# Kernel tuning notes

Hardware: AMD Instinct MI355X
Metric: run time of the kernel (lower is better)

The kernel has to match this reference:

```python
import jax, jax.numpy as jnp
import numpy as np

EPS = 1e-6


def _make_coord_3d(D, H, W, dtype):
    # torch make_coord_3d(flatten=False).permute(3,0,1,2): channels stacked as (x, y, z)
    lz = jnp.linspace(-1.0, 1.0, D, dtype=dtype)
    ly = jnp.linspace(-1.0, 1.0, H, dtype=dtype)
    lx = jnp.linspace(-1.0, 1.0, W, dtype=dtype)
    cz, cy, cx = jnp.meshgrid(lz, ly, lx, indexing='ij')
    return jnp.stack([cx, cy, cz], axis=0)  # [3, D, H, W]


def _trilinear_border(vol, gd, gh, gw):
    # vol: [C, D, H, W]; gd/gh/gw: [Q] normalized coords for the D/H/W axes.
    # Matches torch grid_sample(mode='bilinear', align_corners=False, padding_mode='border').
    C, D, H, W = vol.shape
    z = (gd + 1.0) * (D * 0.5) - 0.5
    y = (gh + 1.0) * (H * 0.5) - 0.5
    x = (gw + 1.0) * (W * 0.5) - 0.5
    z0 = jnp.floor(z); y0 = jnp.floor(y); x0 = jnp.floor(x)
    wz = (z - z0)[None]; wy = (y - y0)[None]; wx = (x - x0)[None]  # [1, Q]
    z0i = jnp.clip(z0.astype(jnp.int32), 0, D - 1); z1i = jnp.clip(z0.astype(jnp.int32) + 1, 0, D - 1)
    y0i = jnp.clip(y0.astype(jnp.int32), 0, H - 1); y1i = jnp.clip(y0.astype(jnp.int32) + 1, 0, H - 1)
    x0i = jnp.clip(x0.astype(jnp.int32), 0, W - 1); x1i = jnp.clip(x0.astype(jnp.int32) + 1, 0, W - 1)
    g = lambda zi, yi, xi: vol[:, zi, yi, xi]  # gather -> [C, Q]
    return (g(z0i, y0i, x0i) * (1 - wz) * (1 - wy) * (1 - wx)
            + g(z0i, y0i, x1i) * (1 - wz) * (1 - wy) * wx
            + g(z0i, y1i, x0i) * (1 - wz) * wy * (1 - wx)
            + g(z0i, y1i, x1i) * (1 - wz) * wy * wx
            + g(z1i, y0i, x0i) * wz * (1 - wy) * (1 - wx)
            + g(z1i, y0i, x1i) * wz * (1 - wy) * wx
            + g(z1i, y1i, x0i) * wz * wy * (1 - wx)
            + g(z1i, y1i, x1i) * wz * wy * wx)


def _forward(inp, coord, cell, W0, b0, W1, b1, W2, b2, W3, b3):
    feat = inp  # identity encoder: inp is the latent feature grid
    B, C, D, H, W = feat.shape
    rx = 2.0 / D / 2.0; ry = 2.0 / H / 2.0; rz = 2.0 / W / 2.0
    sizes = jnp.array([D, H, W], dtype=feat.dtype)
    feat_coord = _make_coord_3d(D, H, W, feat.dtype)  # [3, D, H, W]
    sample_b = jax.vmap(_trilinear_border, in_axes=(0, 0, 0, 0))
    sample_c = jax.vmap(_trilinear_border, in_axes=(None, 0, 0, 0))

    rel_cell = cell * sizes  # [B, Q, 3]
    cell_vol = jnp.abs(cell[..., 0] * cell[..., 1] * cell[..., 2])
    scale_sq = jnp.clip(8.0 / (cell_vol + 1e-8), 1.0, 64.0)[..., None]  # [B, Q, 1]

    def mlp(x):
        h = jax.nn.relu(x @ W0 + b0)
        h = jax.nn.relu(h @ W1 + b1)
        h = jax.nn.relu(h @ W2 + b2)
        return h @ W3 + b3

    preds, areas = [], []
    for vx in (-1, 1):
        for vy in (-1, 1):
            for vz in (-1, 1):
                shift = jnp.array([vx * rx + EPS, vy * ry + EPS, vz * rz + EPS], dtype=coord.dtype)
                c = jnp.clip(coord + shift, -1.0 + 1e-6, 1.0 - 1e-6)
                gd, gh, gw = c[..., 0], c[..., 1], c[..., 2]
                q_feat = sample_b(feat, gd, gh, gw).transpose(0, 2, 1)        # [B, Q, C]
                q_coord = sample_c(feat_coord, gd, gh, gw).transpose(0, 2, 1)  # [B, Q, 3]
                rel_coord = (coord - q_coord) * sizes
                x = jnp.concatenate([q_feat, rel_coord, rel_cell, scale_sq], axis=-1)
                preds.append(mlp(x))  # [B, Q, 1]
                areas.append(jnp.abs(rel_coord[..., 0] * rel_coord[..., 1] * rel_coord[..., 2]) + 1e-9)
    tot_area = jnp.stack(areas).sum(axis=0)
    areas = areas[::-1]  # local-ensemble diagonal-swap of areas
    ret = sum(p * (a / tot_area)[..., None] for p, a in zip(preds, areas))
    return ret


def setup_inputs() -> dict:
    key = jax.random.key(0)
    ks = jax.random.split(key, 8)
    B, C, D, Q, HID = 1, 64, 32, 131072, 256
    in_dim = C + 3 + 3 + 1  # 71
    w = lambda k, shape, fan_in: jax.random.normal(k, shape, jnp.float32) * (1.0 / np.sqrt(fan_in))
    inp = jax.random.normal(ks[0], (B, C, D, D, D), jnp.float32)
    coord = jax.random.uniform(ks[1], (B, Q, 3), jnp.float32, -1.0, 1.0)
    cell = jnp.full((B, Q, 3), 2.0 / 64.0, jnp.float32)  # uniform cell size of a 64^3 query grid
    return {
        'inp': inp, 'coord': coord, 'cell': cell,
        'W0': w(ks[2], (in_dim, HID), in_dim), 'b0': jnp.zeros((HID,), jnp.float32),
        'W1': w(ks[3], (HID, HID), HID), 'b1': jnp.zeros((HID,), jnp.float32),
        'W2': w(ks[4], (HID, HID), HID), 'b2': jnp.zeros((HID,), jnp.float32),
        'W3': w(ks[5], (HID, 1), HID), 'b3': jnp.zeros((1,), jnp.float32),
    }


def reference(inp, coord, cell, W0, b0, W1, b1, W2, b2, W3, b3):
    return _forward(inp, coord, cell, W0, b0, W1, b1, W2, b2, W3, b3)
```

## Files before the change

### kernel.cpp

```cpp
#include <hip/hip_runtime.h>

typedef __attribute__((ext_vector_type(8))) short s16x8;
typedef __attribute__((ext_vector_type(4))) float f32x4;

__device__ __forceinline__ unsigned short f2bf(float x) {
  unsigned u = __float_as_uint(x);
  u = (u + 0x7fffu + ((u >> 16) & 1u)) >> 16;
  return (unsigned short)u;
}
__device__ __forceinline__ float bflo(unsigned v) { return __uint_as_float(v << 16); }
__device__ __forceinline__ float bfhi(unsigned v) { return __uint_as_float(v & 0xffff0000u); }

#define FEAT_OFF 0
#define W0F_OFF  2097152
#define W1F_OFF  (W0F_OFF + 24576)
#define W2F_OFF  (W1F_OFF + 65536)
#define WS_TOTAL (W2F_OFF + 65536)

__global__ void liif_prep(const float* __restrict__ inp,
                          const float* __restrict__ W0,
                          const float* __restrict__ W1,
                          const float* __restrict__ W2,
                          unsigned short* __restrict__ ws) {
  int tid = blockIdx.x * 256 + threadIdx.x;
  if (tid < 2097152) {
    int pos = tid >> 6, c = tid & 63;
    ws[FEAT_OFF + tid] = f2bf(inp[c * 32768 + pos]);
  } else if (tid < W1F_OFF) {
    int e = tid - W0F_OFF;
    int j = e & 7, L = (e >> 3) & 63, nt = (e >> 9) & 15, c = e >> 13;
    int k = c * 32 + (L >> 4) * 8 + j, n = nt * 16 + (L & 15);
    ws[tid] = (k < 71) ? f2bf(W0[k * 256 + n]) : (unsigned short)0;
  } else if (tid < W2F_OFF) {
    int e = tid - W1F_OFF;
    int j = e & 7, L = (e >> 3) & 63, nt = (e >> 9) & 15, c = e >> 13;
    int k = c * 32 + (L >> 4) * 8 + j, n = nt * 16 + (L & 15);
    ws[tid] = f2bf(W1[k * 256 + n]);
  } else if (tid < WS_TOTAL) {
    int e = tid - W2F_OFF;
    int j = e & 7, L = (e >> 3) & 63, nt = (e >> 9) & 15, c = e >> 13;
    int k = c * 32 + (L >> 4) * 8 + j, n = nt * 16 + (L & 15);
    ws[tid] = f2bf(W2[k * 256 + n]);
  }
}

template<int KC>
__device__ __forceinline__ void run_layer(const unsigned short* __restrict__ Wf,
                                          const float* __restrict__ bias,
                                          const unsigned short* A, int astride,
                                          unsigned short* H,
                                          int wave, int quad, int l16, int lane) {
  f32x4 acc[4][4];
#pragma unroll
  for (int i = 0; i < 4; ++i)
#pragma unroll
    for (int j = 0; j < 4; ++j) acc[i][j] = (f32x4){0.f, 0.f, 0.f, 0.f};

#pragma unroll
  for (int c = 0; c < KC; ++c) {
    s16x8 a[4];
#pragma unroll
    for (int rt = 0; rt < 4; ++rt)
      a[rt] = *(const s16x8*)(A + (rt * 16 + l16) * astride + c * 32 + quad * 8);
#pragma unroll
    for (int ntl = 0; ntl < 4; ++ntl) {
      int nt = wave * 4 + ntl;
      s16x8 b = *(const s16x8*)(Wf + (((c * 16 + nt) * 64 + lane) << 3));
#pragma unroll
      for (int rt = 0; rt < 4; ++rt)
        acc[rt][ntl] = __builtin_amdgcn_mfma_f32_16x16x32_bf16(a[rt], b, acc[rt][ntl], 0, 0, 0);
    }
  }
  __syncthreads();
#pragma unroll
  for (int ntl = 0; ntl < 4; ++ntl) {
    int col = (wave * 4 + ntl) * 16 + l16;
    float bv = bias[col];
#pragma unroll
    for (int rt = 0; rt < 4; ++rt) {
#pragma unroll
      for (int i = 0; i < 4; ++i) {
        int r = rt * 16 + quad * 4 + i;
        float h = fmaxf(acc[rt][ntl][i] + bv, 0.0f);
        H[r * 264 + col] = f2bf(h);
      }
    }
  }
  __syncthreads();
}

__global__ __launch_bounds__(256, 3)
void liif_main(const float* __restrict__ coord,
               const float* __restrict__ cell,
               const float* __restrict__ b0,
               const float* __restrict__ b1,
               const float* __restrict__ b2,
               const float* __restrict__ W3,
               const float* __restrict__ b3,
               const unsigned short* __restrict__ ws,
               float* __restrict__ out) {
  __shared__ __align__(16) unsigned short sm_x[64 * 104];
  __shared__ __align__(16) unsigned short sm_h[64 * 264];
  __shared__ float sm_area[64];
  __shared__ float sm_pred[64];

  const unsigned short* feat = ws + FEAT_OFF;
  const int tid = threadIdx.x;
  const int lane = tid & 63;
  const int wave = tid >> 6;
  const int quad = lane >> 4;
  const int l16 = lane & 15;

  {
    const int row = tid >> 2, p = tid & 3;
    const int ql = row >> 3, s = row & 7;
    const int q = blockIdx.x * 8 + ql;
    const float c0r = coord[q * 3 + 0], c1r = coord[q * 3 + 1], c2r = coord[q * 3 + 2];
    const float R = 0.03125f;
    const float sh0 = ((s & 4) ? R : -R) + 1e-6f;
    const float sh1 = ((s & 2) ? R : -R) + 1e-6f;
    const float sh2 = ((s & 1) ? R : -R) + 1e-6f;
    const float LO = -1.0f + 1e-6f, HI = 1.0f - 1e-6f;
    float c0 = fminf(fmaxf(c0r + sh0, LO), HI);
    float c1 = fminf(fmaxf(c1r + sh1, LO), HI);
    float c2 = fminf(fmaxf(c2r + sh2, LO), HI);
    float z = (c0 + 1.0f) * 16.0f - 0.5f;
    float y = (c1 + 1.0f) * 16.0f - 0.5f;
    float x = (c2 + 1.0f) * 16.0f - 0.5f;
    float zf = floorf(z), yf = floorf(y), xf = floorf(x);
    float wz = z - zf, wy = y - yf, wx = x - xf;
    int z0 = min(max((int)zf, 0), 31), z1 = min(max((int)zf + 1, 0), 31);
    int y0 = min(max((int)yf, 0), 31), y1 = min(max((int)yf + 1, 0), 31);
    int x0 = min(max((int)xf, 0), 31), x1 = min(max((int)xf + 1, 0), 31);
    float wz0 = 1.0f - wz, wy0 = 1.0f - wy, wx0 = 1.0f - wx;

    float w[8] = { wz0 * wy0 * wx0, wz0 * wy0 * wx, wz0 * wy * wx0, wz0 * wy * wx,
                   wz  * wy0 * wx0, wz  * wy0 * wx, wz  * wy * wx0, wz  * wy * wx };
    int idx[8] = { (z0 * 32 + y0) * 32 + x0, (z0 * 32 + y0) * 32 + x1,
                   (z0 * 32 + y1) * 32 + x0, (z0 * 32 + y1) * 32 + x1,
                   (z1 * 32 + y0) * 32 + x0, (z1 * 32 + y0) * 32 + x1,
                   (z1 * 32 + y1) * 32 + x0, (z1 * 32 + y1) * 32 + x1 };

    float acc[16];
#pragma unroll
    for (int i = 0; i < 16; ++i) acc[i] = 0.0f;
#pragma unroll
    for (int corner = 0; corner < 8; ++corner) {
      const uint4* cp = (const uint4*)(feat + idx[corner] * 64 + p * 16);
      uint4 v0 = cp[0], v1 = cp[1];
      float wc = w[corner];
      unsigned vv[8] = { v0.x, v0.y, v0.z, v0.w, v1.x, v1.y, v1.z, v1.w };
#pragma unroll
      for (int d = 0; d < 8; ++d) {
        acc[2 * d]     += wc * bflo(vv[d]);
        acc[2 * d + 1] += wc * bfhi(vv[d]);
      }
    }
    unsigned pw[8];
#pragma unroll
    for (int d = 0; d < 8; ++d)
      pw[d] = (unsigned)f2bf(acc[2 * d]) | ((unsigned)f2bf(acc[2 * d + 1]) << 16);
    uint4* dst = (uint4*)(&sm_x[row * 104 + p * 16]);
    dst[0] = make_uint4(pw[0], pw[1], pw[2], pw[3]);
    dst[1] = make_uint4(pw[4], pw[5], pw[6], pw[7]);

    if (p == 0) {
      const float step = 2.0f / 31.0f;
      float qc0 = wx0 * (-1.0f + step * x0) + wx * (-1.0f + step * x1);
      float qc1 = wy0 * (-1.0f + step * y0) + wy * (-1.0f + step * y1);
      float qc2 = wz0 * (-1.0f + step * z0) + wz * (-1.0f + step * z1);
      float rel0 = (c0r - qc0) * 32.0f;
      float rel1 = (c1r - qc1) * 32.0f;
      float rel2 = (c2r - qc2) * 32.0f;
      sm_area[row] = fabsf(rel0 * rel1 * rel2) + 1e-9f;
      float cl0 = cell[q * 3 + 0], cl1 = cell[q * 3 + 1], cl2 = cell[q * 3 + 2];
      float ssq = fminf(fmaxf(8.0f / (fabsf(cl0 * cl1 * cl2) + 1e-8f), 1.0f), 64.0f);
      unsigned tw0 = (unsigned)f2bf(rel0) | ((unsigned)f2bf(rel1) << 16);
      unsigned tw1 = (unsigned)f2bf(rel2) | ((unsigned)f2bf(cl0 * 32.0f) << 16);
      unsigned tw2 = (unsigned)f2bf(cl1 * 32.0f) | ((unsigned)f2bf(cl2 * 32.0f) << 16);
      unsigned tw3 = (unsigned)f2bf(ssq);
      uint4* d2 = (uint4*)(&sm_x[row * 104 + 64]);
      d2[0] = make_uint4(tw0, tw1, tw2, tw3);
      d2[1] = make_uint4(0, 0, 0, 0);
      d2[2] = make_uint4(0, 0, 0, 0);
      d2[3] = make_uint4(0, 0, 0, 0);
    }
  }
  __syncthreads();

  run_layer<3>(ws + W0F_OFF, b0, sm_x, 104, sm_h, wave, quad, l16, lane);
  run_layer<8>(ws + W1F_OFF, b1, sm_h, 264, sm_h, wave, quad, l16, lane);
  run_layer<8>(ws + W2F_OFF, b2, sm_h, 264, sm_h, wave, quad, l16, lane);

  {
    const int row = tid >> 2, p = tid & 3;
    const unsigned short* hp = sm_h + row * 264 + p * 64;
    float sum = 0.0f;
#pragma unroll
    for (int kk = 0; kk < 8; ++kk) {
      const uint4 v = *(const uint4*)(hp + kk * 8);
      const float* w = W3 + p * 64 + kk * 8;
      unsigned vv[4] = { v.x, v.y, v.z, v.w };
#pragma unroll
      for (int d = 0; d < 4; ++d) {
        sum += w[2 * d]     * bflo(vv[d]);
        sum += w[2 * d + 1] * bfhi(vv[d]);
      }
    }
    sum += __shfl_xor(sum, 1);
    sum += __shfl_xor(sum, 2);
    if (p == 0) sm_pred[row] = sum + b3[0];
  }
  __syncthreads();

  if (tid < 8) {
    const int ql = tid;
    float tot = 0.0f, ret = 0.0f;
#pragma unroll
    for (int s = 0; s < 8; ++s) tot += sm_area[ql * 8 + s];
#pragma unroll
    for (int s = 0; s < 8; ++s) ret += sm_pred[ql * 8 + s] * sm_area[ql * 8 + (7 - s)];
    out[blockIdx.x * 8 + ql] = ret / tot;
  }
}

extern "C" void kernel_launch(void* const* d_in, const int* in_sizes, int n_in,
                              void* d_out, int out_size, void* d_ws, size_t ws_size,
                              hipStream_t stream) {
  const float* inp   = (const float*)d_in[0];
  const float* coord = (const float*)d_in[1];
  const float* cell  = (const float*)d_in[2];
  const float* W0    = (const float*)d_in[3];
  const float* b0    = (const float*)d_in[4];
  const float* W1    = (const float*)d_in[5];
  const float* b1    = (const float*)d_in[6];
  const float* W2    = (const float*)d_in[7];
  const float* b2    = (const float*)d_in[8];
  const float* W3    = (const float*)d_in[9];
  const float* b3    = (const float*)d_in[10];
  unsigned short* ws = (unsigned short*)d_ws;
  float* out = (float*)d_out;

  const int Q = in_sizes[1] / 3;
  hipLaunchKernelGGL(liif_prep, dim3((WS_TOTAL + 255) / 256), dim3(256), 0, stream,
                     inp, W0, W1, W2, ws);
  hipLaunchKernelGGL(liif_main, dim3(Q / 8), dim3(256), 0, stream,
                     coord, cell, b0, b1, b2, W3, b3, ws, out);
}
```

Baseline: 495.1 us.

## Merge LDS buffers, raise occupancy, tile-transpose prep, use packed bf16 convert

Merges the input and hidden LDS buffers into one 64x260 array so each block uses less shared memory, and raises the launch-bounds occupancy hint from 3 to 4 blocks per SM. The prep kernel's feature transpose now goes through an LDS tile so both the global reads and writes are coalesced. Float-to-bf16 packing uses the hardware packed-convert builtin when it exists. Risks: higher register pressure under the tighter launch bound, possible bank conflicts from the new 260 stride, and rounding that may differ slightly from the manual conversion.

Result: slower. 792.2 us (+60.0%).

```diff
diff --git a/kernel.cpp b/kernel.cpp
--- a/kernel.cpp
+++ b/kernel.cpp
@@ -7,6 +7,14 @@
   unsigned u = __float_as_uint(x);
   u = (u + 0x7fffu + ((u >> 16) & 1u)) >> 16;
   return (unsigned short)u;
+}
+__device__ __forceinline__ unsigned cvtpk(float a, float b) {
+#if __has_builtin(__builtin_amdgcn_cvt_pk_bf16_f32)
+  auto t = __builtin_amdgcn_cvt_pk_bf16_f32(a, b);
+  return __builtin_bit_cast(unsigned, t);
+#else
+  return (unsigned)f2bf(a) | ((unsigned)f2bf(b) << 16);
+#endif
 }
 __device__ __forceinline__ float bflo(unsigned v) { return __uint_as_float(v << 16); }
 __device__ __forceinline__ float bfhi(unsigned v) { return __uint_as_float(v & 0xffff0000u); }
@@ -17,37 +25,54 @@
 #define W2F_OFF  (W1F_OFF + 65536)
 #define WS_TOTAL (W2F_OFF + 65536)
 
+#define HSTR 260
+
 __global__ void liif_prep(const float* __restrict__ inp,
                           const float* __restrict__ W0,
                           const float* __restrict__ W1,
                           const float* __restrict__ W2,
                           unsigned short* __restrict__ ws) {
-  int tid = blockIdx.x * 256 + threadIdx.x;
-  if (tid < 2097152) {
-    int pos = tid >> 6, c = tid & 63;
-    ws[FEAT_OFF + tid] = f2bf(inp[c * 32768 + pos]);
-  } else if (tid < W1F_OFF) {
-    int e = tid - W0F_OFF;
-    int j = e & 7, L = (e >> 3) & 63, nt = (e >> 9) & 15, c = e >> 13;
-    int k = c * 32 + (L >> 4) * 8 + j, n = nt * 16 + (L & 15);
-    ws[tid] = (k < 71) ? f2bf(W0[k * 256 + n]) : (unsigned short)0;
-  } else if (tid < W2F_OFF) {
-    int e = tid - W1F_OFF;
-    int j = e & 7, L = (e >> 3) & 63, nt = (e >> 9) & 15, c = e >> 13;
-    int k = c * 32 + (L >> 4) * 8 + j, n = nt * 16 + (L & 15);
-    ws[tid] = f2bf(W1[k * 256 + n]);
-  } else if (tid < WS_TOTAL) {
-    int e = tid - W2F_OFF;
-    int j = e & 7, L = (e >> 3) & 63, nt = (e >> 9) & 15, c = e >> 13;
-    int k = c * 32 + (L >> 4) * 8 + j, n = nt * 16 + (L & 15);
-    ws[tid] = f2bf(W2[k * 256 + n]);
+  const int b = blockIdx.x;
+  if (b < 512) {
+    __shared__ unsigned short tile[64][68];
+    const int pos0 = b * 64;
+    const int w = threadIdx.x >> 6, lane = threadIdx.x & 63;
+#pragma unroll
+    for (int ci = 0; ci < 16; ++ci) {
+      int c = w * 16 + ci;
+      tile[lane][c] = f2bf(inp[c * 32768 + pos0 + lane]);
+    }
+    __syncthreads();
+#pragma unroll
+    for (int pi = 0; pi < 16; ++pi) {
+      int p = w * 16 + pi;
+      ws[FEAT_OFF + (pos0 + p) * 64 + lane] = tile[p][lane];
+    }
+  } else {
+    int tid = (b - 512) * 256 + (int)threadIdx.x + W0F_OFF;
+    if (tid < W1F_OFF) {
+      int e = tid - W0F_OFF;
+      int j = e & 7, L = (e >> 3) & 63, nt = (e >> 9) & 15, c = e >> 13;
+      int k = c * 32 + (L >> 4) * 8 + j, n = nt * 16 + (L & 15);
+      ws[tid] = (k < 71) ? f2bf(W0[k * 256 + n]) : (unsigned short)0;
+    } else if (tid < W2F_OFF) {
+      int e = tid - W1F_OFF;
+      int j = e & 7, L = (e >> 3) & 63, nt = (e >> 9) & 15, c = e >> 13;
+      int k = c * 32 + (L >> 4) * 8 + j, n = nt * 16 + (L & 15);
+      ws[tid] = f2bf(W1[k * 256 + n]);
+    } else if (tid < WS_TOTAL) {
+      int e = tid - W2F_OFF;
+      int j = e & 7, L = (e >> 3) & 63, nt = (e >> 9) & 15, c = e >> 13;
+      int k = c * 32 + (L >> 4) * 8 + j, n = nt * 16 + (L & 15);
+      ws[tid] = f2bf(W2[k * 256 + n]);
+    }
   }
 }
 
 template<int KC>
 __device__ __forceinline__ void run_layer(const unsigned short* __restrict__ Wf,
                                           const float* __restrict__ bias,
-                                          const unsigned short* A, int astride,
+                                          const unsigned short* A,
                                           unsigned short* H,
                                           int wave, int quad, int l16, int lane) {
   f32x4 acc[4][4];
@@ -61,7 +86,7 @@
     s16x8 a[4];
 #pragma unroll
     for (int rt = 0; rt < 4; ++rt)
-      a[rt] = *(const s16x8*)(A + (rt * 16 + l16) * astride + c * 32 + quad * 8);
+      a[rt] = *(const s16x8*)(A + (rt * 16 + l16) * HSTR + c * 32 + quad * 8);
 #pragma unroll
     for (int ntl = 0; ntl < 4; ++ntl) {
       int nt = wave * 4 + ntl;
@@ -78,18 +103,21 @@
     float bv = bias[col];
 #pragma unroll
     for (int rt = 0; rt < 4; ++rt) {
-#pragma unroll
-      for (int i = 0; i < 4; ++i) {
-        int r = rt * 16 + quad * 4 + i;
-        float h = fmaxf(acc[rt][ntl][i] + bv, 0.0f);
-        H[r * 264 + col] = f2bf(h);
+      int r0 = rt * 16 + quad * 4;
+#pragma unroll
+      for (int i = 0; i < 4; i += 2) {
+        float h0 = fmaxf(acc[rt][ntl][i] + bv, 0.0f);
+        float h1 = fmaxf(acc[rt][ntl][i + 1] + bv, 0.0f);
+        unsigned pk = cvtpk(h0, h1);
+        H[(r0 + i) * HSTR + col]     = (unsigned short)pk;
+        H[(r0 + i + 1) * HSTR + col] = (unsigned short)(pk >> 16);
       }
     }
   }
   __syncthreads();
 }
 
-__global__ __launch_bounds__(256, 3)
+__global__ __launch_bounds__(256, 4)
 void liif_main(const float* __restrict__ coord,
                const float* __restrict__ cell,
                const float* __restrict__ b0,
@@ -99,8 +127,7 @@
                const float* __restrict__ b3,
                const unsigned short* __restrict__ ws,
                float* __restrict__ out) {
-  __shared__ __align__(16) unsigned short sm_x[64 * 104];
-  __shared__ __align__(16) unsigned short sm_h[64 * 264];
+  __shared__ __align__(16) unsigned short sm[64 * HSTR];
   __shared__ float sm_area[64];
   __shared__ float sm_pred[64];
 
@@ -158,9 +185,8 @@
     }
     unsigned pw[8];
 #pragma unroll
-    for (int d = 0; d < 8; ++d)
-      pw[d] = (unsigned)f2bf(acc[2 * d]) | ((unsigned)f2bf(acc[2 * d + 1]) << 16);
-    uint4* dst = (uint4*)(&sm_x[row * 104 + p * 16]);
+    for (int d = 0; d < 8; ++d) pw[d] = cvtpk(acc[2 * d], acc[2 * d + 1]);
+    uint4* dst = (uint4*)(&sm[row * HSTR + p * 16]);
     dst[0] = make_uint4(pw[0], pw[1], pw[2], pw[3]);
     dst[1] = make_uint4(pw[4], pw[5], pw[6], pw[7]);
 
@@ -175,11 +201,11 @@
       sm_area[row] = fabsf(rel0 * rel1 * rel2) + 1e-9f;
       float cl0 = cell[q * 3 + 0], cl1 = cell[q * 3 + 1], cl2 = cell[q * 3 + 2];
       float ssq = fminf(fmaxf(8.0f / (fabsf(cl0 * cl1 * cl2) + 1e-8f), 1.0f), 64.0f);
-      unsigned tw0 = (unsigned)f2bf(rel0) | ((unsigned)f2bf(rel1) << 16);
-      unsigned tw1 = (unsigned)f2bf(rel2) | ((unsigned)f2bf(cl0 * 32.0f) << 16);
-      unsigned tw2 = (unsigned)f2bf(cl1 * 32.0f) | ((unsigned)f2bf(cl2 * 32.0f) << 16);
-      unsigned tw3 = (unsigned)f2bf(ssq);
-      uint4* d2 = (uint4*)(&sm_x[row * 104 + 64]);
+      unsigned tw0 = cvtpk(rel0, rel1);
+      unsigned tw1 = cvtpk(rel2, cl0 * 32.0f);
+      unsigned tw2 = cvtpk(cl1 * 32.0f, cl2 * 32.0f);
+      unsigned tw3 = cvtpk(ssq, 0.0f);
+      uint4* d2 = (uint4*)(&sm[row * HSTR + 64]);
       d2[0] = make_uint4(tw0, tw1, tw2, tw3);
       d2[1] = make_uint4(0, 0, 0, 0);
       d2[2] = make_uint4(0, 0, 0, 0);
@@ -188,13 +214,13 @@
   }
   __syncthreads();
 
-  run_layer<3>(ws + W0F_OFF, b0, sm_x, 104, sm_h, wave, quad, l16, lane);
-  run_layer<8>(ws + W1F_OFF, b1, sm_h, 264, sm_h, wave, quad, l16, lane);
-  run_layer<8>(ws + W2F_OFF, b2, sm_h, 264, sm_h, wave, quad, l16, lane);
+  run_layer<3>(ws + W0F_OFF, b0, sm, sm, wave, quad, l16, lane);
+  run_layer<8>(ws + W1F_OFF, b1, sm, sm, wave, quad, l16, lane);
+  run_layer<8>(ws + W2F_OFF, b2, sm, sm, wave, quad, l16, lane);
 
   {
     const int row = tid >> 2, p = tid & 3;
-    const unsigned short* hp = sm_h + row * 264 + p * 64;
+    const unsigned short* hp = sm + row * HSTR + p * 64;
     float sum = 0.0f;
 #pragma unroll
     for (int kk = 0; kk < 8; ++kk) {
@@ -242,7 +268,8 @@
   float* out = (float*)d_out;
 
   const int Q = in_sizes[1] / 3;
-  hipLaunchKernelGGL(liif_prep, dim3((WS_TOTAL + 255) / 256), dim3(256), 0, stream,
+  const int wblocks = (WS_TOTAL - W0F_OFF + 255) / 256;
+  hipLaunchKernelGGL(liif_prep, dim3(512 + wblocks), dim3(256), 0, stream,
                      inp, W0, W1, W2, ws);
   hipLaunchKernelGGL(liif_main, dim3(Q / 8), dim3(256), 0, stream,
                      coord, cell, b0, b1, b2, W3, b3, ws, out);
```
